# Optimization experiments

Measured on AMD Instinct MI355X. Metric: run time of the kernel, lower is better.

## Reference

```python
import jax, jax.numpy as jnp
import numpy as np

B, E, C, H = 128, 512, 128, 8
D = E // H
K = 21  # kNN neighbors per electrode (min(21, C))


def setup_inputs() -> dict:
    key = jax.random.key(0)
    ks = jax.random.split(key, 7)
    x = jax.random.normal(ks[0], (B, E, C), dtype=jnp.float32)
    # 1x1 Conv1d with no bias == [E_out, E_in] matmul over the feature dim
    wq = jax.random.normal(ks[1], (E, E), dtype=jnp.float32) * (E ** -0.5)
    wk = jax.random.normal(ks[2], (E, E), dtype=jnp.float32) * (E ** -0.5)
    wv = jax.random.normal(ks[3], (E, E), dtype=jnp.float32) * (E ** -0.5)
    wo = jax.random.normal(ks[4], (E, E), dtype=jnp.float32) * (E ** -0.5)
    dir_vec = jax.random.normal(ks[5], (H, C), dtype=jnp.float32)

    # synthetic electrode positions (stands in for electrode_positions.pt)
    pos = jax.random.normal(ks[6], (C, 3), dtype=jnp.float32)

    # arc_dist: great-circle distance scaled by mean radius
    radii = jnp.linalg.norm(pos, axis=1, keepdims=True)
    posn = pos / radii
    dist = jnp.arccos(jnp.clip(posn @ posn.T, -1.0, 1.0)) * radii.mean()

    # Gaussian spatial bias, row-mean centered
    sigma = jnp.median(jnp.tril(dist, 1))
    attn_bias = -dist ** 2 / (2.0 * sigma ** 2 + 1e-8)
    attn_bias = attn_bias - attn_bias.mean(axis=1, keepdims=True)

    # unit displacement vectors, zeroed on the diagonal: disp[i,j] = unit(pos[j]-pos[i])
    disp = pos[None, :, :] - pos[:, None, :]
    disp = disp / jnp.clip(jnp.linalg.norm(disp, axis=-1, keepdims=True), 1e-8)
    disp = disp.at[jnp.arange(C), jnp.arange(C)].set(0.0)

    # kNN mask: K smallest distances per row (includes self)
    _, knn_idx = jax.lax.top_k(-dist, K)
    knn_mask = jnp.zeros((C, C), dtype=bool).at[jnp.arange(C)[:, None], knn_idx].set(True)

    return {"x": x, "wq": wq, "wk": wk, "wv": wv, "wo": wo,
            "dir_vec": dir_vec, "attn_bias": attn_bias,
            "displacement": disp, "knn_mask": knn_mask}


def reference(x, wq, wk, wv, wo, dir_vec, attn_bias, displacement, knn_mask):
    scale = D ** -0.5
    # q/k/v projections: 1x1 conv (no bias) + SELU, then split heads -> [B,H,D,C]
    q = jax.nn.selu(jnp.einsum('oe,bec->boc', wq, x)).reshape(B, H, D, C)
    k = jax.nn.selu(jnp.einsum('oe,bec->boc', wk, x)).reshape(B, H, D, C)
    v = jax.nn.selu(jnp.einsum('oe,bec->boc', wv, x)).reshape(B, H, D, C)

    # scores[b,h,i,j] = <q[...,i], k[...,j]> * scale + spatial bias
    scores = jnp.einsum('bhdi,bhdj->bhij', q, k) * scale + attn_bias[None, None]

    # per-head antisymmetric directional bias
    dvn = dir_vec / jnp.clip(jnp.linalg.norm(dir_vec, axis=-1, keepdims=True), 1e-12)
    dir_bias = displacement.mean(axis=-1)[None, :, :] * dvn[:, None, :]  # [H,C,C]
    dir_bias = 0.5 * (dir_bias - jnp.swapaxes(dir_bias, -1, -2))
    scores = scores + (dir_bias - dir_bias.mean(axis=-1, keepdims=True))[None]

    # kNN masking + stable softmax
    scores = jnp.where(knn_mask[None, None], scores, -jnp.inf)
    scores = scores - scores.max(axis=-1, keepdims=True)
    p = jax.nn.softmax(scores, axis=-1)

    # aggregate values and merge heads -> [B, E, C]
    attn = jnp.einsum('bhij,bhdj->bhdi', p, v).reshape(B, E, C)
    # output projection (AlphaDropout is identity in eval)
    return jax.nn.selu(jnp.einsum('oe,bec->boc', wo, attn))
```

## Files before the change

### kernel.cpp

```cpp
#include <hip/hip_runtime.h>
#include <math.h>

#define B_ 128
#define E_ 512
#define C_ 128
#define H_ 8
#define D_ 64
#define BEC_ ((size_t)B_ * E_ * C_)

typedef __attribute__((ext_vector_type(8))) __bf16 bf16x8;
typedef __attribute__((ext_vector_type(4))) float f32x4;

__device__ __forceinline__ ushort f2bf(float f) {
    unsigned u = __float_as_uint(f);
    unsigned r = u + 0x7fffu + ((u >> 16) & 1u);
    return (ushort)(r >> 16);
}
__device__ __forceinline__ float bf2f(ushort h) {
    return __uint_as_float(((unsigned)h) << 16);
}
__device__ __forceinline__ void split_bf(float f, ushort& hi, ushort& lo) {
    hi = f2bf(f);
    lo = f2bf(f - bf2f(hi));
}
__device__ __forceinline__ float selu_f(float x) {
    const float alpha = 1.6732632423543772f;
    const float scale = 1.0507009873554805f;
    return x > 0.0f ? scale * x : scale * alpha * expm1f(x);
}
__device__ __forceinline__ void gll16(const void* g, void* l) {
    __builtin_amdgcn_global_load_lds(
        (const __attribute__((address_space(1))) void*)g,
        (__attribute__((address_space(3))) void*)l, 16, 0, 0);
}

__global__ void detect_mask_kernel(const unsigned char* __restrict__ m,
                                   int* __restrict__ flag) {
    __shared__ int cnt;
    if (threadIdx.x == 0) cnt = 0;
    __syncthreads();
    int local = 0;
    for (int i = threadIdx.x; i < C_ * C_; i += blockDim.x) local += (m[i] != 0);
    atomicAdd(&cnt, local);
    __syncthreads();
    if (threadIdx.x == 0) *flag = (cnt > 1600) ? 1 : 0;
}

__global__ __launch_bounds__(128) void bias_prep_kernel(
    const float* __restrict__ dir_vec, const float* __restrict__ attn_bias,
    const float* __restrict__ disp, const unsigned char* __restrict__ maskb,
    const int* __restrict__ flag, float* __restrict__ combT)
{
    const int i = blockIdx.x, h = blockIdx.y, j = threadIdx.x;
    __shared__ float red[128];

    float dv = dir_vec[h * C_ + j];
    red[j] = dv * dv;
    __syncthreads();
    for (int s = 64; s > 0; s >>= 1) {
        if (j < s) red[j] += red[j + s];
        __syncthreads();
    }
    const float nrm = fmaxf(sqrtf(red[0]), 1e-12f);
    __syncthreads();

    const float dvn_j = dir_vec[h * C_ + j] / nrm;
    const float dvn_i = dir_vec[h * C_ + i] / nrm;
    const float third = 1.0f / 3.0f;
    const float dm_ij = (disp[(i * C_ + j) * 3 + 0] + disp[(i * C_ + j) * 3 + 1] +
                         disp[(i * C_ + j) * 3 + 2]) * third;
    const float dm_ji = (disp[(j * C_ + i) * 3 + 0] + disp[(j * C_ + i) * 3 + 1] +
                         disp[(j * C_ + i) * 3 + 2]) * third;
    const float db = 0.5f * (dm_ij * dvn_j - dm_ji * dvn_i);

    red[j] = db;
    __syncthreads();
    for (int s = 64; s > 0; s >>= 1) {
        if (j < s) red[j] += red[j + s];
        __syncthreads();
    }
    const float rowmean = red[0] * (1.0f / 128.0f);

    const bool mk = (*flag) ? (maskb[i * C_ + j] != 0)
                            : (((const int*)maskb)[i * C_ + j] != 0);
    combT[((size_t)h * C_ + j) * C_ + i] =
        mk ? (attn_bias[i * C_ + j] + db - rowmean) : -INFINITY;
}

__global__ __launch_bounds__(256) void wsplit_kernel(
    const float* __restrict__ w0, const float* __restrict__ w1,
    const float* __restrict__ w2, const float* __restrict__ w3,
    ushort* __restrict__ wh, ushort* __restrict__ wl)
{
    const int s = blockIdx.y;
    const float* __restrict__ w = (s == 0) ? w0 : (s == 1) ? w1 : (s == 2) ? w2 : w3;
    const size_t base = (size_t)s * E_ * E_;
    const size_t i0 = ((size_t)blockIdx.x * 256 + threadIdx.x) * 8;
    const float4 f0 = *(const float4*)&w[i0];
    const float4 f1 = *(const float4*)&w[i0 + 4];
    const float ff[8] = {f0.x, f0.y, f0.z, f0.w, f1.x, f1.y, f1.z, f1.w};
    union { ushort u[8]; uint4 v; } hu, lu;
#pragma unroll
    for (int j = 0; j < 8; ++j) split_bf(ff[j], hu.u[j], lu.u[j]);
    *(uint4*)&wh[base + i0] = hu.v;
    *(uint4*)&wl[base + i0] = lu.v;
}

__global__ __launch_bounds__(256) void xsplit_kernel(
    const float* __restrict__ x, ushort* __restrict__ xh, ushort* __restrict__ xl)
{
    const int b = blockIdx.y, e0 = blockIdx.x * 64;
    __shared__ float ts[64][132];
    const int tid = threadIdx.x;
    const float* __restrict__ xb = x + ((size_t)b * E_ + e0) * C_;
#pragma unroll
    for (int r = 0; r < 8; ++r) {
        const int idx = tid + r * 256;
        const int e = idx >> 5, c4 = idx & 31;
        *(float4*)&ts[e][c4 * 4] = *(const float4*)&xb[(size_t)e * C_ + c4 * 4];
    }
    __syncthreads();
    const int lc = tid >> 3;
    const int l8 = (tid & 7) * 8;
#pragma unroll
    for (int p = 0; p < 4; ++p) {
        const int c = p * 32 + lc;
        union { ushort u[8]; uint4 v; } hu, lu;
#pragma unroll
        for (int j = 0; j < 8; ++j) split_bf(ts[l8 + j][c], hu.u[j], lu.u[j]);
        const size_t rb = ((size_t)b * C_ + c) * E_ + e0 + l8;
        *(uint4*)&xh[rb] = hu.v;
        *(uint4*)&xl[rb] = lu.v;
    }
}

template<int MODE>
__global__ __launch_bounds__(256, 2) void gemm_kernel(
    const ushort* __restrict__ Wh0, const ushort* __restrict__ Wh1,
    const ushort* __restrict__ Wh2, const ushort* __restrict__ Wl0,
    const ushort* __restrict__ Wl1, const ushort* __restrict__ Wl2,
    const ushort* __restrict__ Bh, const ushort* __restrict__ Bl,
    ushort* __restrict__ qh, ushort* __restrict__ ql,
    ushort* __restrict__ kh, ushort* __restrict__ kl,
    ushort* __restrict__ vhp, float* __restrict__ fout)
{
    const int d = blockIdx.x;
    const int xr = d & 7, slot = d >> 3;
    const int G = (MODE == 0) ? 12 : 4;
    const int b = xr + 8 * (slot / G);
    const int u = slot % G;
    const int z = (MODE == 0) ? (u >> 2) : 0;
    const int o0 = (MODE == 0) ? ((u & 3) * 128) : (u * 128);

    const ushort* __restrict__ wh = (z == 0) ? Wh0 : (z == 1) ? Wh1 : Wh2;
    const ushort* __restrict__ wl = (z == 0) ? Wl0 : (z == 1) ? Wl1 : Wl2;
    const bool trans = (MODE == 0) && (z < 2);

    __shared__ ushort sm[4 * 8192];

    const int tid = threadIdx.x;
    const int wid = tid >> 6, lane = tid & 63;
    const int wr64 = (wid >> 1) * 64, wc64 = (wid & 1) * 64;
    const int w4 = wid * 4;
    const int srow = lane >> 3;
    const size_t gco = (size_t)((lane & 7) ^ srow) * 16;

    const char* __restrict__ bhp = (const char*)(Bh + (size_t)b * C_ * E_);
    const char* __restrict__ blp = (const char*)(Bl + (size_t)b * C_ * E_);
    const char* __restrict__ whp = (const char*)wh;
    const char* __restrict__ wlp = (const char*)wl;

    const char* __restrict__ smb = (const char*)sm;
    const int aoffB = trans ? 32768 : 0;
    const int boffB = trans ? 0 : 32768;

    f32x4 acc[4][4];
#pragma unroll
    for (int m = 0; m < 4; ++m)
#pragma unroll
        for (int n = 0; n < 4; ++n) acc[m][n] = (f32x4)0.0f;

    const int l15 = lane & 15;

    for (int k0 = 0; k0 < E_; k0 += 64) {
#pragma unroll
        for (int t = 0; t < 4; ++t) {
            const int inst = w4 + t;
            const int r = inst * 8 + srow;
            const size_t arow = ((size_t)(o0 + r) * E_ + k0) * 2 + gco;
            const size_t brow = ((size_t)r * E_ + k0) * 2 + gco;
            gll16(whp + arow, &sm[inst * 512]);
            gll16(wlp + arow, &sm[8192 + inst * 512]);
            gll16(bhp + brow, &sm[16384 + inst * 512]);
            gll16(blp + brow, &sm[24576 + inst * 512]);
        }
        __syncthreads();
#pragma unroll
        for (int kk = 0; kk < 2; ++kk) {
            const int kbyte = kk * 64 + (lane >> 4) * 16;
            bf16x8 ah[4], al[4], bh4[4], bl4[4];
#pragma unroll
            for (int m = 0; m < 4; ++m) {
                const int r = wr64 + m * 16 + l15;
                const int byt = r * 128 + (kbyte ^ ((r & 7) << 4));
                ah[m] = *(const bf16x8*)(smb + aoffB + byt);
                al[m] = *(const bf16x8*)(smb + aoffB + 16384 + byt);
            }
#pragma unroll
            for (int n = 0; n < 4; ++n) {
                const int c = wc64 + n * 16 + l15;
                const int byt = c * 128 + (kbyte ^ ((c & 7) << 4));
                bh4[n] = *(const bf16x8*)(smb + boffB + byt);
                bl4[n] = *(const bf16x8*)(smb + boffB + 16384 + byt);
            }
#pragma unroll
            for (int m = 0; m < 4; ++m)
#pragma unroll
                for (int n = 0; n < 4; ++n)
                    acc[m][n] = __builtin_amdgcn_mfma_f32_16x16x32_bf16(
                        ah[m], bh4[n], acc[m][n], 0, 0, 0);
#pragma unroll
            for (int m = 0; m < 4; ++m)
#pragma unroll
                for (int n = 0; n < 4; ++n)
                    acc[m][n] = __builtin_amdgcn_mfma_f32_16x16x32_bf16(
                        ah[m], bl4[n], acc[m][n], 0, 0, 0);
#pragma unroll
            for (int m = 0; m < 4; ++m)
#pragma unroll
                for (int n = 0; n < 4; ++n)
                    acc[m][n] = __builtin_amdgcn_mfma_f32_16x16x32_bf16(
                        al[m], bh4[n], acc[m][n], 0, 0, 0);
        }
        __syncthreads();
    }

    const int lr = (lane >> 4) * 4, lc = lane & 15;
    if (MODE == 1) {
        float* __restrict__ outb = fout + (size_t)b * E_ * C_;
#pragma unroll
        for (int m = 0; m < 4; ++m)
#pragma unroll
            for (int n = 0; n < 4; ++n) {
                float* po = outb + (size_t)(o0 + wr64 + m * 16 + lr) * C_ +
                            wc64 + n * 16 + lc;
                const f32x4 a = acc[m][n];
#pragma unroll
                for (int j = 0; j < 4; ++j) po[(size_t)j * C_] = selu_f(a[j]);
            }
    } else if (z == 2) {
#pragma unroll
        for (int m = 0; m < 4; ++m)
#pragma unroll
            for (int n = 0; n < 4; ++n) {
                const f32x4 a = acc[m][n];
#pragma unroll
                for (int j = 0; j < 4; ++j) {
                    const size_t idx = ((size_t)b * E_ + o0 + wr64 + m * 16 + lr + j) * C_ +
                                       wc64 + n * 16 + lc;
                    vhp[idx] = f2bf(selu_f(a[j]));
                }
            }
    } else {
        ushort* __restrict__ th = z ? kh : qh;
        ushort* __restrict__ tl = z ? kl : ql;
#pragma unroll
        for (int m = 0; m < 4; ++m)
#pragma unroll
            for (int n = 0; n < 4; ++n) {
                const f32x4 a = acc[m][n];
#pragma unroll
                for (int j = 0; j < 4; ++j) {
                    const int c = wr64 + m * 16 + lr + j;
                    const int o = o0 + wc64 + n * 16 + lc;
                    const size_t idx = ((size_t)b * C_ + c) * E_ + o;
                    ushort hi, lo;
                    split_bf(selu_f(a[j]), hi, lo);
                    th[idx] = hi;
                    tl[idx] = lo;
                }
            }
    }
}

__global__ __launch_bounds__(256, 2) void attn_mfma_kernel(
    const ushort* __restrict__ qTh, const ushort* __restrict__ qTl,
    const ushort* __restrict__ kTh, const ushort* __restrict__ kTl,
    const ushort* __restrict__ vh,  const float* __restrict__ combT,
    ushort* __restrict__ aTh, ushort* __restrict__ aTl)
{
    const int dd_ = blockIdx.x;
    const int b = (dd_ & 7) + 8 * ((dd_ >> 3) >> 3);
    const int h = (dd_ >> 3) & 7;
    __shared__ ushort lds[40960];
    ushort* sQh = lds;
    ushort* sQl = lds + 8192;
    ushort* sKh = lds + 16384;
    ushort* sKl = lds + 24576;
    ushort* sV  = lds + 32768;
    ushort* sPh = lds;
    ushort* sPl = lds + 16384;

    const int tid = threadIdx.x, wid = tid >> 6, lane = tid & 63;

    {
        const size_t gq = (size_t)b * C_ * E_ + h * D_;
        const int rsub = lane >> 3, chunk = lane & 7;
#pragma unroll
        for (int t = 0; t < 4; ++t) {
            const int inst = wid * 4 + t;
            const int row = inst * 8 + rsub;
            const size_t goff = (gq + (size_t)row * E_) * 2 +
                                (size_t)(chunk ^ (row & 7)) * 16;
            gll16((const char*)qTh + goff, &sQh[inst * 512]);
            gll16((const char*)qTl + goff, &sQl[inst * 512]);
            gll16((const char*)kTh + goff, &sKh[inst * 512]);
            gll16((const char*)kTl + goff, &sKl[inst * 512]);
        }
        const size_t gv = ((size_t)b * E_ + h * D_) * C_;
        const int vr = lane >> 4, vchunk = lane & 15;
#pragma unroll
        for (int t = 0; t < 4; ++t) {
            const int inst = wid * 4 + t;
            const int row = inst * 4 + vr;
            const size_t goff = (gv + (size_t)row * C_) * 2 +
                                (size_t)(vchunk ^ (row & 7)) * 16;
            gll16((const char*)vh + goff, &sV[inst * 512]);
        }
    }
    __syncthreads();

    const int i0 = wid * 32;
    const int l15 = lane & 15;

    f32x4 acc[2][8];
#pragma unroll
    for (int m = 0; m < 2; ++m)
#pragma unroll
        for (int n = 0; n < 8; ++n) acc[m][n] = (f32x4)0.0f;

#pragma unroll
    for (int kk = 0; kk < 2; ++kk) {
        const int kbyte = kk * 64 + (lane >> 4) * 16;
        bf16x8 qhf[2], qlf[2];
#pragma unroll
        for (int m = 0; m < 2; ++m) {
            const int r = i0 + m * 16 + l15;
            const int byt = r * 128 + (kbyte ^ ((r & 7) << 4));
            qhf[m] = *(const bf16x8*)((const char*)sQh + byt);
            qlf[m] = *(const bf16x8*)((const char*)sQl + byt);
        }
#pragma unroll
        for (int n = 0; n < 8; ++n) {
            const int r = n * 16 + l15;
            const int byt = r * 128 + (kbyte ^ ((r & 7) << 4));
            const bf16x8 khf = *(const bf16x8*)((const char*)sKh + byt);
            const bf16x8 klf = *(const bf16x8*)((const char*)sKl + byt);
#pragma unroll
            for (int m = 0; m < 2; ++m) {
                acc[m][n] = __builtin_amdgcn_mfma_f32_16x16x32_bf16(
                    qhf[m], khf, acc[m][n], 0, 0, 0);
                acc[m][n] = __builtin_amdgcn_mfma_f32_16x16x32_bf16(
                    qhf[m], klf, acc[m][n], 0, 0, 0);
                acc[m][n] = __builtin_amdgcn_mfma_f32_16x16x32_bf16(
                    qlf[m], khf, acc[m][n], 0, 0, 0);
            }
        }
    }

#pragma unroll
    for (int m = 0; m < 2; ++m)
#pragma unroll
        for (int n = 0; n < 8; ++n) {
            const int jcol = n * 16 + l15;
            const float4 cb = *(const float4*)&combT[
                ((size_t)h * C_ + jcol) * C_ + i0 + m * 16 + (lane >> 4) * 4];
            acc[m][n][0] = fmaf(acc[m][n][0], 0.125f, cb.x);
            acc[m][n][1] = fmaf(acc[m][n][1], 0.125f, cb.y);
            acc[m][n][2] = fmaf(acc[m][n][2], 0.125f, cb.z);
            acc[m][n][3] = fmaf(acc[m][n][3], 0.125f, cb.w);
        }

#pragma unroll
    for (int m = 0; m < 2; ++m)
#pragma unroll
        for (int jj = 0; jj < 4; ++jj) {
            float mx = -INFINITY;
#pragma unroll
            for (int n = 0; n < 8; ++n) mx = fmaxf(mx, acc[m][n][jj]);
#pragma unroll
            for (int off = 1; off < 16; off <<= 1)
                mx = fmaxf(mx, __shfl_xor(mx, off));
            float sum = 0.0f;
#pragma unroll
            for (int n = 0; n < 8; ++n) {
                const float e = __expf(acc[m][n][jj] - mx);
                acc[m][n][jj] = e;
                sum += e;
            }
#pragma unroll
            for (int off = 1; off < 16; off <<= 1) sum += __shfl_xor(sum, off);
            const float inv = 1.0f / sum;
#pragma unroll
            for (int n = 0; n < 8; ++n) acc[m][n][jj] *= inv;
        }

    __syncthreads();
#pragma unroll
    for (int m = 0; m < 2; ++m)
#pragma unroll
        for (int n = 0; n < 8; ++n)
#pragma unroll
            for (int jj = 0; jj < 4; ++jj) {
                const int i = i0 + m * 16 + (lane >> 4) * 4 + jj;
                const int col = n * 16 + l15;
                const int byt = i * 256 + ((col * 2) ^ ((i & 7) << 4));
                ushort hi, lo;
                split_bf(acc[m][n][jj], hi, lo);
                *(ushort*)((char*)sPh + byt) = hi;
                *(ushort*)((char*)sPl + byt) = lo;
            }
    __syncthreads();

    f32x4 acc2[2][4];
#pragma unroll
    for (int m = 0; m < 2; ++m)
#pragma unroll
        for (int n = 0; n < 4; ++n) acc2[m][n] = (f32x4)0.0f;

#pragma unroll
    for (int ks = 0; ks < 4; ++ks) {
        const int kbyte = ks * 64 + (lane >> 4) * 16;
        bf16x8 ph[2], pl[2];
#pragma unroll
        for (int m = 0; m < 2; ++m) {
            const int r = i0 + m * 16 + l15;
            const int byt = r * 256 + (kbyte ^ ((r & 7) << 4));
            ph[m] = *(const bf16x8*)((const char*)sPh + byt);
            pl[m] = *(const bf16x8*)((const char*)sPl + byt);
        }
#pragma unroll
        for (int n = 0; n < 4; ++n) {
            const int d = n * 16 + l15;
            const int byt = d * 256 + (kbyte ^ ((d & 7) << 4));
            const bf16x8 vb = *(const bf16x8*)((const char*)sV + byt);
#pragma unroll
            for (int m = 0; m < 2; ++m) {
                acc2[m][n] = __builtin_amdgcn_mfma_f32_16x16x32_bf16(
                    ph[m], vb, acc2[m][n], 0, 0, 0);
                acc2[m][n] = __builtin_amdgcn_mfma_f32_16x16x32_bf16(
                    pl[m], vb, acc2[m][n], 0, 0, 0);
            }
        }
    }

#pragma unroll
    for (int m = 0; m < 2; ++m)
#pragma unroll
        for (int n = 0; n < 4; ++n)
#pragma unroll
            for (int jj = 0; jj < 4; ++jj) {
                const int i = i0 + m * 16 + (lane >> 4) * 4 + jj;
                const int dcol = n * 16 + l15;
                ushort hi, lo;
                split_bf(acc2[m][n][jj], hi, lo);
                const size_t idx = ((size_t)b * C_ + i) * E_ + h * D_ + dcol;
                aTh[idx] = hi;
                aTl[idx] = lo;
            }
}

extern "C" void kernel_launch(void* const* d_in, const int* in_sizes, int n_in,
                              void* d_out, int out_size, void* d_ws, size_t ws_size,
                              hipStream_t stream) {
    const float* x        = (const float*)d_in[0];
    const float* wq       = (const float*)d_in[1];
    const float* wk       = (const float*)d_in[2];
    const float* wv       = (const float*)d_in[3];
    const float* wo       = (const float*)d_in[4];
    const float* dir_vec  = (const float*)d_in[5];
    const float* attn_b   = (const float*)d_in[6];
    const float* disp     = (const float*)d_in[7];
    const unsigned char* knn = (const unsigned char*)d_in[8];
    float* out = (float*)d_out;

    char* ws = (char*)d_ws;
    size_t off = 0;
    ushort* qTh = (ushort*)(ws + off); off += BEC_ * 2;
    ushort* qTl = (ushort*)(ws + off); off += BEC_ * 2;
    ushort* kTh = (ushort*)(ws + off); off += BEC_ * 2;
    ushort* kTl = (ushort*)(ws + off); off += BEC_ * 2;
    ushort* vbuf = (ushort*)(ws + off); off += BEC_ * 2;
    ushort* xTh = (ushort*)(ws + off); off += BEC_ * 2;
    ushort* xTl = (ushort*)(ws + off); off += BEC_ * 2;
    ushort* wh  = (ushort*)(ws + off); off += (size_t)4 * E_ * E_ * 2;
    ushort* wl  = (ushort*)(ws + off); off += (size_t)4 * E_ * E_ * 2;
    float* combT = (float*)(ws + off); off += (size_t)H_ * C_ * C_ * sizeof(float);
    int* flag = (int*)(ws + off);

    detect_mask_kernel<<<1, 256, 0, stream>>>(knn, flag);
    bias_prep_kernel<<<dim3(C_, H_), 128, 0, stream>>>(dir_vec, attn_b, disp, knn,
                                                       flag, combT);
    wsplit_kernel<<<dim3(128, 4), 256, 0, stream>>>(wq, wk, wv, wo, wh, wl);
    xsplit_kernel<<<dim3(8, B_), 256, 0, stream>>>(x, xTh, xTl);

    const size_t WSZ = (size_t)E_ * E_;
    gemm_kernel<0><<<1536, 256, 0, stream>>>(
        wh, wh + WSZ, wh + 2 * WSZ, wl, wl + WSZ, wl + 2 * WSZ,
        xTh, xTl, qTh, qTl, kTh, kTl, vbuf, nullptr);
    attn_mfma_kernel<<<1024, 256, 0, stream>>>(
        qTh, qTl, kTh, kTl, vbuf, combT, xTh, xTl);
    gemm_kernel<1><<<512, 256, 0, stream>>>(
        wh + 3 * WSZ, wh + 3 * WSZ, wh + 3 * WSZ,
        wl + 3 * WSZ, wl + 3 * WSZ, wl + 3 * WSZ,
        xTh, xTl, nullptr, nullptr, nullptr, nullptr, nullptr, out);
}
```

Baseline: 197.8 us.

## Fuse mask detection and split kernels, drop low-weight term for V projection

Moves the mask-format detection into bias_prep (each block counts the first 2048 bytes itself) and merges the weight and x bf16 split kernels into a single launch, cutting two kernel launches. It also skips the weight-low × x-high MFMA term and its load for the V projection (z==2), which reduces V's precision from three-term to two-term split-bf16. The shortcut trades accuracy on V for fewer MFMAs and less global traffic, and the per-block mask count adds redundant work in bias_prep.

Measured after the change: 176.0 us (median of 3 runs). -11.0%, faster.

```diff
diff --git a/kernel.cpp b/kernel.cpp
--- a/kernel.cpp
+++ b/kernel.cpp
@@ -34,25 +34,29 @@
         (__attribute__((address_space(3))) void*)l, 16, 0, 0);
 }
 
-__global__ void detect_mask_kernel(const unsigned char* __restrict__ m,
-                                   int* __restrict__ flag) {
-    __shared__ int cnt;
-    if (threadIdx.x == 0) cnt = 0;
-    __syncthreads();
-    int local = 0;
-    for (int i = threadIdx.x; i < C_ * C_; i += blockDim.x) local += (m[i] != 0);
-    atomicAdd(&cnt, local);
-    __syncthreads();
-    if (threadIdx.x == 0) *flag = (cnt > 1600) ? 1 : 0;
-}
-
 __global__ __launch_bounds__(128) void bias_prep_kernel(
     const float* __restrict__ dir_vec, const float* __restrict__ attn_bias,
     const float* __restrict__ disp, const unsigned char* __restrict__ maskb,
-    const int* __restrict__ flag, float* __restrict__ combT)
+    float* __restrict__ combT)
 {
     const int i = blockIdx.x, h = blockIdx.y, j = threadIdx.x;
     __shared__ float red[128];
+    __shared__ int boolFlag;
+
+    {
+        int cnt = 0;
+        const int base = j * 16;
+#pragma unroll
+        for (int t = 0; t < 16; ++t) cnt += (maskb[base + t] != 0);
+        red[j] = (float)cnt;
+        __syncthreads();
+        for (int s = 64; s > 0; s >>= 1) {
+            if (j < s) red[j] += red[j + s];
+            __syncthreads();
+        }
+        if (j == 0) boolFlag = (red[0] > 200.0f) ? 1 : 0;
+        __syncthreads();
+    }
 
     float dv = dir_vec[h * C_ + j];
     red[j] = dv * dv;
@@ -81,37 +85,42 @@
     }
     const float rowmean = red[0] * (1.0f / 128.0f);
 
-    const bool mk = (*flag) ? (maskb[i * C_ + j] != 0)
-                            : (((const int*)maskb)[i * C_ + j] != 0);
+    const bool mk = boolFlag ? (maskb[i * C_ + j] != 0)
+                             : (((const int*)maskb)[i * C_ + j] != 0);
     combT[((size_t)h * C_ + j) * C_ + i] =
         mk ? (attn_bias[i * C_ + j] + db - rowmean) : -INFINITY;
 }
 
-__global__ __launch_bounds__(256) void wsplit_kernel(
+__global__ __launch_bounds__(256) void split_kernel(
     const float* __restrict__ w0, const float* __restrict__ w1,
     const float* __restrict__ w2, const float* __restrict__ w3,
-    ushort* __restrict__ wh, ushort* __restrict__ wl)
+    const float* __restrict__ x,
+    ushort* __restrict__ wh, ushort* __restrict__ wl,
+    ushort* __restrict__ xh, ushort* __restrict__ xl)
 {
-    const int s = blockIdx.y;
-    const float* __restrict__ w = (s == 0) ? w0 : (s == 1) ? w1 : (s == 2) ? w2 : w3;
-    const size_t base = (size_t)s * E_ * E_;
-    const size_t i0 = ((size_t)blockIdx.x * 256 + threadIdx.x) * 8;
-    const float4 f0 = *(const float4*)&w[i0];
-    const float4 f1 = *(const float4*)&w[i0 + 4];
-    const float ff[8] = {f0.x, f0.y, f0.z, f0.w, f1.x, f1.y, f1.z, f1.w};
-    union { ushort u[8]; uint4 v; } hu, lu;
-#pragma unroll
-    for (int j = 0; j < 8; ++j) split_bf(ff[j], hu.u[j], lu.u[j]);
-    *(uint4*)&wh[base + i0] = hu.v;
-    *(uint4*)&wl[base + i0] = lu.v;
-}
-
-__global__ __launch_bounds__(256) void xsplit_kernel(
-    const float* __restrict__ x, ushort* __restrict__ xh, ushort* __restrict__ xl)
-{
-    const int b = blockIdx.y, e0 = blockIdx.x * 64;
     __shared__ float ts[64][132];
+    const int id = blockIdx.x;
     const int tid = threadIdx.x;
+
+    if (id < 512) {
+        const int s = id >> 7;
+        const float* __restrict__ w = (s == 0) ? w0 : (s == 1) ? w1
+                                    : (s == 2) ? w2 : w3;
+        const size_t base = (size_t)s * E_ * E_;
+        const size_t i0 = ((size_t)(id & 127) * 256 + tid) * 8;
+        const float4 f0 = *(const float4*)&w[i0];
+        const float4 f1 = *(const float4*)&w[i0 + 4];
+        const float ff[8] = {f0.x, f0.y, f0.z, f0.w, f1.x, f1.y, f1.z, f1.w};
+        union { ushort u[8]; uint4 v; } hu, lu;
+#pragma unroll
+        for (int j = 0; j < 8; ++j) split_bf(ff[j], hu.u[j], lu.u[j]);
+        *(uint4*)&wh[base + i0] = hu.v;
+        *(uint4*)&wl[base + i0] = lu.v;
+        return;
+    }
+
+    const int fid = id - 512;
+    const int b = fid >> 3, e0 = (fid & 7) * 64;
     const float* __restrict__ xb = x + ((size_t)b * E_ + e0) * C_;
 #pragma unroll
     for (int r = 0; r < 8; ++r) {
@@ -155,6 +164,7 @@
     const ushort* __restrict__ wh = (z == 0) ? Wh0 : (z == 1) ? Wh1 : Wh2;
     const ushort* __restrict__ wl = (z == 0) ? Wl0 : (z == 1) ? Wl1 : Wl2;
     const bool trans = (MODE == 0) && (z < 2);
+    const bool full3 = (MODE == 1) || (z != 2);
 
     __shared__ ushort sm[4 * 8192];
 
@@ -190,7 +200,7 @@
             const size_t arow = ((size_t)(o0 + r) * E_ + k0) * 2 + gco;
             const size_t brow = ((size_t)r * E_ + k0) * 2 + gco;
             gll16(whp + arow, &sm[inst * 512]);
-            gll16(wlp + arow, &sm[8192 + inst * 512]);
+            if (full3) gll16(wlp + arow, &sm[8192 + inst * 512]);
             gll16(bhp + brow, &sm[16384 + inst * 512]);
             gll16(blp + brow, &sm[24576 + inst * 512]);
         }
@@ -204,7 +214,7 @@
                 const int r = wr64 + m * 16 + l15;
                 const int byt = r * 128 + (kbyte ^ ((r & 7) << 4));
                 ah[m] = *(const bf16x8*)(smb + aoffB + byt);
-                al[m] = *(const bf16x8*)(smb + aoffB + 16384 + byt);
+                if (full3) al[m] = *(const bf16x8*)(smb + aoffB + 16384 + byt);
             }
 #pragma unroll
             for (int n = 0; n < 4; ++n) {
@@ -225,12 +235,14 @@
                 for (int n = 0; n < 4; ++n)
                     acc[m][n] = __builtin_amdgcn_mfma_f32_16x16x32_bf16(
                         ah[m], bl4[n], acc[m][n], 0, 0, 0);
-#pragma unroll
-            for (int m = 0; m < 4; ++m)
-#pragma unroll
-                for (int n = 0; n < 4; ++n)
-                    acc[m][n] = __builtin_amdgcn_mfma_f32_16x16x32_bf16(
-                        al[m], bh4[n], acc[m][n], 0, 0, 0);
+            if (full3) {
+#pragma unroll
+                for (int m = 0; m < 4; ++m)
+#pragma unroll
+                    for (int n = 0; n < 4; ++n)
+                        acc[m][n] = __builtin_amdgcn_mfma_f32_16x16x32_bf16(
+                            al[m], bh4[n], acc[m][n], 0, 0, 0);
+            }
         }
         __syncthreads();
     }
@@ -441,8 +453,8 @@
         }
 #pragma unroll
         for (int n = 0; n < 4; ++n) {
-            const int d = n * 16 + l15;
-            const int byt = d * 256 + (kbyte ^ ((d & 7) << 4));
+            const int dcol = n * 16 + l15;
+            const int byt = dcol * 256 + (kbyte ^ ((dcol & 7) << 4));
             const bf16x8 vb = *(const bf16x8*)((const char*)sV + byt);
 #pragma unroll
             for (int m = 0; m < 2; ++m) {
@@ -496,13 +508,10 @@
     ushort* wh  = (ushort*)(ws + off); off += (size_t)4 * E_ * E_ * 2;
     ushort* wl  = (ushort*)(ws + off); off += (size_t)4 * E_ * E_ * 2;
     float* combT = (float*)(ws + off); off += (size_t)H_ * C_ * C_ * sizeof(float);
-    int* flag = (int*)(ws + off);
-
-    detect_mask_kernel<<<1, 256, 0, stream>>>(knn, flag);
-    bias_prep_kernel<<<dim3(C_, H_), 128, 0, stream>>>(dir_vec, attn_b, disp, knn,
-                                                       flag, combT);
-    wsplit_kernel<<<dim3(128, 4), 256, 0, stream>>>(wq, wk, wv, wo, wh, wl);
-    xsplit_kernel<<<dim3(8, B_), 256, 0, stream>>>(x, xTh, xTl);
+
+    bias_prep_kernel<<<dim3(C_, H_), 128, 0, stream>>>(dir_vec, attn_b, disp,
+                                                       knn, combT);
+    split_kernel<<<1536, 256, 0, stream>>>(wq, wk, wv, wo, x, wh, wl, xTh, xTl);
 
     const size_t WSZ = (size_t)E_ * E_;
     gemm_kernel<0><<<1536, 256, 0, stream>>>(
```
